# Kernel optimization log

Hardware: AMD Instinct MI355X
Metric: run time of the kernel (lower is better)

## Reference

```python
import jax, jax.numpy as jnp
import numpy as np
from jax.scipy.special import logsumexp

B, T, V, E, H, K = 64, 512, 21128, 256, 512, 31


def setup_inputs() -> dict:
    key = jax.random.key(0)
    ks = jax.random.split(key, 32)
    s = 1.0 / np.sqrt(H)

    def u(k, shape):
        return jax.random.uniform(k, shape, jnp.float32, -s, s)

    inp = {
        "input_ids": jax.random.randint(ks[0], (B, T), 0, V),
        "labels": jax.random.randint(ks[1], (B, T), 0, K),
        "emb": jax.random.normal(ks[2], (V, E), jnp.float32) * 0.05,
    }
    i = 3
    for layer, insz in (("l0", E), ("l1", 2 * H)):
        for d in ("f", "b"):
            inp["w_ih_%s%s" % (layer, d)] = u(ks[i], (3 * H, insz)); i += 1
            inp["w_hh_%s%s" % (layer, d)] = u(ks[i], (3 * H, H)); i += 1
            inp["b_ih_%s%s" % (layer, d)] = u(ks[i], (3 * H,)); i += 1
            inp["b_hh_%s%s" % (layer, d)] = u(ks[i], (3 * H,)); i += 1
    inp["cls_w"] = u(ks[i], (K, 2 * H))
    inp["cls_b"] = u(ks[i + 1], (K,))
    inp["crf_start"] = jax.random.normal(ks[i + 2], (K,), jnp.float32) * 0.1
    inp["crf_end"] = jax.random.normal(ks[i + 3], (K,), jnp.float32) * 0.1
    inp["crf_trans"] = jax.random.normal(ks[i + 4], (K, K), jnp.float32) * 0.1
    return inp


def gru_dir(x, w_ih, w_hh, b_ih, b_hh, reverse):
    # x: [B, T, in]. PyTorch GRU gate math, gates ordered (r, z, n).
    xp = jnp.einsum('bti,gi->btg', x, w_ih) + b_ih  # [B, T, 3H] precomputed input gates
    if reverse:
        xp = xp[:, ::-1]
    h0 = jnp.zeros((x.shape[0], w_hh.shape[1]), x.dtype)

    def step(h, xt):
        gh = h @ w_hh.T + b_hh
        xr, xz, xn = jnp.split(xt, 3, axis=-1)
        hr, hz, hn = jnp.split(gh, 3, axis=-1)
        r = jax.nn.sigmoid(xr + hr)
        z = jax.nn.sigmoid(xz + hz)
        n = jnp.tanh(xn + r * hn)
        h_new = (1.0 - z) * n + z * h
        return h_new, h_new

    _, hs = jax.lax.scan(step, h0, jnp.swapaxes(xp, 0, 1))
    hs = jnp.swapaxes(hs, 0, 1)  # [B, T, H]
    if reverse:
        hs = hs[:, ::-1]
    return hs


def crf_llh(emissions, tags, mask, start, end, trans):
    # Linear-chain CRF log-likelihood, summed over batch. mask[:, 0] assumed True.
    Bn = emissions.shape[0]
    mf = mask.astype(emissions.dtype)
    bidx = jnp.arange(Bn)
    em_t = jnp.take_along_axis(emissions, tags[:, :, None], axis=2)[:, :, 0]  # [B, T]
    num = start[tags[:, 0]] + em_t[:, 0]
    tr = trans[tags[:, :-1], tags[:, 1:]]  # [B, T-1]
    num = num + jnp.sum((tr + em_t[:, 1:]) * mf[:, 1:], axis=1)
    last_idx = jnp.sum(mask.astype(jnp.int32), axis=1) - 1
    num = num + end[tags[bidx, last_idx]]

    alpha0 = start[None, :] + emissions[:, 0]  # [B, K]

    def step(alpha, inp):
        em, m = inp  # em [B, K], m [B]
        nxt = logsumexp(alpha[:, :, None] + trans[None] + em[:, None, :], axis=1)
        return jnp.where(m[:, None], nxt, alpha), None

    alpha, _ = jax.lax.scan(
        step, alpha0,
        (jnp.swapaxes(emissions[:, 1:], 0, 1), jnp.swapaxes(mask[:, 1:], 0, 1)))
    denom = logsumexp(alpha + end[None, :], axis=1)
    return jnp.sum(num - denom)


def reference(input_ids, labels, emb,
              w_ih_l0f, w_hh_l0f, b_ih_l0f, b_hh_l0f,
              w_ih_l0b, w_hh_l0b, b_ih_l0b, b_hh_l0b,
              w_ih_l1f, w_hh_l1f, b_ih_l1f, b_hh_l1f,
              w_ih_l1b, w_hh_l1b, b_ih_l1b, b_hh_l1b,
              cls_w, cls_b, crf_start, crf_end, crf_trans):
    x = emb[input_ids]  # [B, T, E]
    f0 = gru_dir(x, w_ih_l0f, w_hh_l0f, b_ih_l0f, b_hh_l0f, False)
    b0 = gru_dir(x, w_ih_l0b, w_hh_l0b, b_ih_l0b, b_hh_l0b, True)
    h1 = jnp.concatenate([f0, b0], axis=-1)  # [B, T, 2H]
    f1 = gru_dir(h1, w_ih_l1f, w_hh_l1f, b_ih_l1f, b_hh_l1f, False)
    b1 = gru_dir(h1, w_ih_l1b, w_hh_l1b, b_ih_l1b, b_hh_l1b, True)
    gru_out = jnp.concatenate([f1, b1], axis=-1)  # [B, T, 2H]
    emissions = jnp.einsum('bth,kh->btk', gru_out, cls_w) + cls_b  # [B, T, K]
    mask = labels > -1  # labels.gt(labels_padding_value=-1)
    loss = -crf_llh(emissions, labels, mask, crf_start, crf_end, crf_trans)
    return (loss, emissions)
```

## Files before the change

kernel.cpp:

```cpp
#include <hip/hip_runtime.h>

#define DI __device__ __forceinline__

constexpr int B_  = 64;
constexpr int T_  = 512;
constexpr int E_  = 256;
constexpr int H_  = 512;
constexpr int G_  = 1536;
constexpr int H2_ = 1024;
constexpr int K_  = 31;
constexpr int BT_ = B_ * T_;
constexpr int TC_ = 64;
constexpr int NC_ = T_ / TC_;

typedef float        f32x4  __attribute__((ext_vector_type(4)));
typedef short        bf16x8 __attribute__((ext_vector_type(8)));
typedef unsigned int u32x4  __attribute__((ext_vector_type(4)));
typedef unsigned long long ull;

DI float bf2f(unsigned short u) {
    union { unsigned int i; float f; } v; v.i = ((unsigned int)u) << 16; return v.f;
}
DI unsigned short f2bf(float f) {
    union { float f; unsigned int i; } v; v.f = f;
    unsigned int r = v.i + 0x7fffu + ((v.i >> 16) & 1u);
    return (unsigned short)(r >> 16);
}
DI float sigm(float x) { return 1.f / (1.f + __expf(-x)); }
DI float tanh_(float x) {
    x = fminf(15.f, fmaxf(-15.f, x));
    float e = __expf(-2.f * x);
    return (1.f - e) / (1.f + e);
}

#define MFMA16(a, b, c) __builtin_amdgcn_mfma_f32_16x16x32_bf16(a, b, c, 0, 0, 0)

__global__ void cvt_f32_bf16(const float* __restrict__ src, unsigned short* __restrict__ dst, int n) {
    int i = blockIdx.x * blockDim.x + threadIdx.x;
    int stride = gridDim.x * blockDim.x;
    for (; i < n; i += stride) dst[i] = f2bf(src[i]);
}

__global__ __launch_bounds__(256) void cvt_cls(const float* __restrict__ src,
                                               unsigned short* __restrict__ dstf,
                                               unsigned short* __restrict__ dstb) {
    int i = blockIdx.x * 256 + threadIdx.x;
    if (i >= 32 * H_) return;
    int n = i >> 9, k = i & 511;
    float vf = (n < K_) ? src[n * H2_ + k] : 0.f;
    float vb = (n < K_) ? src[n * H2_ + H_ + k] : 0.f;
    dstf[i] = f2bf(vf);
    dstb[i] = f2bf(vb);
}

__global__ __launch_bounds__(256) void emis_bias_init(const float* __restrict__ cls_b,
                                                      float* __restrict__ out1) {
    int i = blockIdx.x * 256 + threadIdx.x;
    int stride = gridDim.x * 256;
    for (; i < BT_ * K_; i += stride) {
        int n = i - (i / K_) * K_;
        out1[i] = cls_b[n];
    }
}

template <bool OUTF32, bool ACCUM, bool WF32, bool AGATHER>
DI void gemm_tile(unsigned short (*As)[40], unsigned short (*Ws)[40],
                  const unsigned short* A, const float* gsrc, const int* ids, int lda,
                  size_t arow0, const void* W, int ldw, int nrows, int n0,
                  const float* bias, void* Cout, int ldc, size_t crow0,
                  int nout, int ksz, int tid) {
    const int w = tid >> 6, l = tid & 63;
    const int srow = tid >> 2, sc8 = (tid & 3) * 8;
    const int mw = (w >> 1) * 32, nw = (w & 1) * 32;
    const int fl = l & 15, fk = (l >> 4) * 8;
    f32x4 z4 = { 0.f, 0.f, 0.f, 0.f };
    f32x4 acc[2][2];
    acc[0][0] = z4; acc[0][1] = z4; acc[1][0] = z4; acc[1][1] = z4;
    size_t abase;
    if (AGATHER) abase = (size_t)ids[arow0 + srow] * lda;
    else         abase = (arow0 + srow) * (size_t)lda;

    for (int kc = 0; kc < ksz; kc += 32) {
        u32x4 av, wvv;
        if (AGATHER) {
            const float4* ap = (const float4*)(gsrc + abase + kc + sc8);
            float4 a0 = ap[0], a1 = ap[1];
            union { unsigned short s[8]; u32x4 v; } r;
            r.s[0] = f2bf(a0.x); r.s[1] = f2bf(a0.y); r.s[2] = f2bf(a0.z); r.s[3] = f2bf(a0.w);
            r.s[4] = f2bf(a1.x); r.s[5] = f2bf(a1.y); r.s[6] = f2bf(a1.z); r.s[7] = f2bf(a1.w);
            av = r.v;
        } else {
            av = *(const u32x4*)(A + abase + kc + sc8);
        }
        if (WF32) {
            const float4* wp = (const float4*)((const float*)W + (size_t)(n0 + srow) * ldw + kc + sc8);
            float4 w0 = wp[0], w1 = wp[1];
            union { unsigned short s[8]; u32x4 v; } r;
            r.s[0] = f2bf(w0.x); r.s[1] = f2bf(w0.y); r.s[2] = f2bf(w0.z); r.s[3] = f2bf(w0.w);
            r.s[4] = f2bf(w1.x); r.s[5] = f2bf(w1.y); r.s[6] = f2bf(w1.z); r.s[7] = f2bf(w1.w);
            wvv = r.v;
        } else {
            if (n0 + srow < nrows)
                wvv = *(const u32x4*)((const unsigned short*)W + (size_t)(n0 + srow) * ldw + kc + sc8);
            else { u32x4 zz = { 0u, 0u, 0u, 0u }; wvv = zz; }
        }
        __syncthreads();
        *(u32x4*)&As[srow][sc8] = av;
        *(u32x4*)&Ws[srow][sc8] = wvv;
        __syncthreads();
        bf16x8 a0 = *(const bf16x8*)&As[mw + fl][fk];
        bf16x8 a1 = *(const bf16x8*)&As[mw + 16 + fl][fk];
        bf16x8 b0 = *(const bf16x8*)&Ws[nw + fl][fk];
        bf16x8 b1 = *(const bf16x8*)&Ws[nw + 16 + fl][fk];
        acc[0][0] = MFMA16(a0, b0, acc[0][0]);
        acc[0][1] = MFMA16(a0, b1, acc[0][1]);
        acc[1][0] = MFMA16(a1, b0, acc[1][0]);
        acc[1][1] = MFMA16(a1, b1, acc[1][1]);
    }

    #pragma unroll
    for (int mf = 0; mf < 2; ++mf)
        #pragma unroll
        for (int nf = 0; nf < 2; ++nf) {
            int col = n0 + nw + nf * 16 + fl;
            if (col >= nout) continue;
            float bv = bias ? bias[col] : 0.f;
            #pragma unroll
            for (int j = 0; j < 4; ++j) {
                int r = mw + mf * 16 + (l >> 4) * 4 + j;
                size_t crow = crow0 + r;
                float v = acc[mf][nf][j] + bv;
                if (OUTF32) {
                    float* C = (float*)Cout;
                    if (ACCUM) C[crow * ldc + col] += v;
                    else       C[crow * ldc + col] = v;
                } else {
                    ((unsigned short*)Cout)[crow * ldc + col] = f2bf(v);
                }
            }
        }
}

template <bool OUTF32, bool ACCUM, bool WF32, bool AGATHER>
__global__ __launch_bounds__(256) void gemm_k(
        const unsigned short* __restrict__ A, const float* __restrict__ gsrc,
        const int* __restrict__ ids, int lda, int m_base, int astride,
        const void* __restrict__ W, int ldw, int nrows,
        const float* __restrict__ bias,
        void* __restrict__ Cout, int ldc, int c_base, int cstride, int nout, int ksz) {
    __shared__ unsigned short As[64][40];
    __shared__ unsigned short Ws[64][40];
    gemm_tile<OUTF32, ACCUM, WF32, AGATHER>(As, Ws, A, gsrc, ids, lda,
        (size_t)m_base + (size_t)blockIdx.x * astride, W, ldw, nrows,
        blockIdx.y * 64, bias, Cout, ldc,
        (size_t)c_base + (size_t)blockIdx.x * cstride, nout, ksz, threadIdx.x);
}

__global__ __launch_bounds__(256) void emis_k(
        const unsigned short* __restrict__ gof, const unsigned short* __restrict__ gob,
        const unsigned short* __restrict__ clsf, const unsigned short* __restrict__ clsb,
        float* __restrict__ out1, int t0f, int t0b) {
    __shared__ unsigned short As[64][40];
    __shared__ unsigned short Ws[64][40];
    const unsigned short* A = blockIdx.y ? gob : gof;
    const unsigned short* W = blockIdx.y ? clsb : clsf;
    int t0 = blockIdx.y ? t0b : t0f;
    gemm_tile<true, true, false, false>(As, Ws, A, nullptr, nullptr, H_,
        (size_t)blockIdx.x * TC_, W, H_, 32, 0, nullptr,
        (void*)out1, K_, (size_t)t0 + (size_t)blockIdx.x * T_, K_, H_, threadIdx.x);
}

template <bool AGATHER>
__global__ __launch_bounds__(256, 1) void fused_scan_gemm(
        int c, int layer,
        const unsigned short* __restrict__ xpc_f, const unsigned short* __restrict__ xpc_b,
        const unsigned short* __restrict__ whh_f, const unsigned short* __restrict__ whh_b,
        const float* __restrict__ bhh_f, const float* __restrict__ bhh_b,
        unsigned int* __restrict__ hpub,
        float* __restrict__ hcar,
        unsigned short* __restrict__ out_f, unsigned short* __restrict__ out_b,
        int ldo, int mode, int* __restrict__ flags,
        const unsigned short* __restrict__ gA, const float* __restrict__ gsrc,
        const int* __restrict__ gids, int glda,
        const float* __restrict__ gwf, const float* __restrict__ gwb,
        const float* __restrict__ gbf, const float* __restrict__ gbb,
        unsigned short* __restrict__ xpf_nxt, unsigned short* __restrict__ xpb_nxt,
        int t0f_n, int t0b_n, int do_gemm) {
    __shared__ unsigned short As[64][40];
    __shared__ unsigned short Ws[64][40];
    __shared__ unsigned short hs[16 * 512];
    const int bid = blockIdx.x;
    const int tid = threadIdx.x;

    if (bid >= 64) {
        if (!do_gemm) return;
        const int gb = bid - 64;
        for (int job = gb; job < 2 * 64 * 24; job += 192) {
            int dirj = job & 1;
            int rest = job >> 1;
            int mt = rest & 63;
            int nt = rest >> 6;
            const float* gw = dirj ? gwb : gwf;
            const float* gbias = dirj ? gbb : gbf;
            unsigned short* gout = dirj ? xpb_nxt : xpf_nxt;
            int t0 = dirj ? t0b_n : t0f_n;
            gemm_tile<false, false, true, AGATHER>(As, Ws, gA, gsrc, gids, glda,
                (size_t)t0 + (size_t)mt * T_, gw, glda, G_, nt * 64, gbias,
                (void*)gout, G_, (size_t)mt * TC_, G_, glda, tid);
        }
        return;
    }

    const int dir = bid >> 5;
    const int rb  = bid & 31;
    const int ug  = rb >> 2;
    const int bg  = rb & 3;
    const int w = tid >> 6, l = tid & 63;
    const int fl = l & 15, q = l >> 4, fko = q * 8;
    const unsigned short* xp = dir ? xpc_b : xpc_f;
    const unsigned short* whh = dir ? whh_b : whh_f;
    const float* bhh = dir ? bhh_b : bhh_f;
    unsigned short* outp = dir ? out_b : out_f;
    int* pollb  = flags + (dir * 4 + bg) * 8 * 32;
    int* myflag = pollb + ug * 32;

    const int u0w = ug * 64 + w * 16;
    bf16x8 wv[3][16];
    #pragma unroll
    for (int g = 0; g < 3; ++g)
        #pragma unroll
        for (int ks = 0; ks < 16; ++ks)
            wv[g][ks] = *(const bf16x8*)(whh + (size_t)(g * H_ + u0w + fl) * H_ + ks * 32 + fko);

    const int u = u0w + fl;
    const float br_ = bhh[u], bz_ = bhh[H_ + u], bn_ = bhh[2 * H_ + u];
    const int mb = bg * 16 + q * 4;
    const int srowl = tid >> 4;
    const int sseg  = tid & 15;

    float hp[4];
    if (c > 0) {
        #pragma unroll
        for (int j = 0; j < 4; ++j) hp[j] = hcar[dir * (B_ * H_) + (mb + j) * H_ + u];
    } else {
        #pragma unroll
        for (int j = 0; j < 4; ++j) hp[j] = 0.f;
    }

    unsigned short xg[3][4];
    auto ldxp = [&](int tl) {
        #pragma unroll
        for (int j = 0; j < 4; ++j) {
            const unsigned short* xb = xp + ((size_t)((mb + j) * TC_ + tl) * G_) + u;
            xg[0][j] = xb[0]; xg[1][j] = xb[H_]; xg[2][j] = xb[2 * H_];
        }
    };
    ldxp(dir ? (TC_ - 1) : 0);

    for (int sl = 0; sl < TC_; ++sl) {
        const int s  = c * TC_ + sl;
        const int gs = layer * T_ + s;
        const int t = dir ? (T_ - 1 - s) : s;
        const int tloc = dir ? (TC_ - 1 - sl) : sl;

        f32x4 z4 = { 0.f, 0.f, 0.f, 0.f };
        f32x4 acc[3];
        acc[0] = z4; acc[1] = z4; acc[2] = z4;

        if (s > 0) {
            if (sl > 0) {
                int v = gs;
                if (l < 8) v = __hip_atomic_load(pollb + l * 32, __ATOMIC_RELAXED, __HIP_MEMORY_SCOPE_AGENT);
                while (!__all(v >= gs)) {
                    __builtin_amdgcn_s_sleep(1);
                    if (l < 8) v = __hip_atomic_load(pollb + l * 32, __ATOMIC_RELAXED, __HIP_MEMORY_SCOPE_AGENT);
                }
                asm volatile("" ::: "memory");
            }
            {
                const ull* src = (const ull*)(hpub
                    + ((size_t)((((s - 1) & 1) * 2 + dir) * B_ + bg * 16 + srowl)) * 256)
                    + sseg * 8;
                ull qv[8];
                #pragma unroll
                for (int i = 0; i < 8; ++i)
                    qv[i] = __hip_atomic_load(src + i, __ATOMIC_RELAXED, __HIP_MEMORY_SCOPE_AGENT);
                char* dst = (char*)hs + srowl * 1024;
                #pragma unroll
                for (int i = 0; i < 4; ++i) {
                    unsigned int byt = (unsigned int)(sseg * 64 + i * 16);
                    byt ^= ((unsigned int)(srowl & 7)) << 4;
                    union { ull qq[2]; u32x4 v4; } pk;
                    pk.qq[0] = qv[2 * i]; pk.qq[1] = qv[2 * i + 1];
                    *(u32x4*)(dst + byt) = pk.v4;
                }
            }
            __syncthreads();
            #pragma unroll
            for (int ks = 0; ks < 16; ++ks) {
                unsigned int byt = (unsigned int)(ks * 64 + q * 16);
                byt ^= ((unsigned int)(fl & 7)) << 4;
                bf16x8 afr = *(const bf16x8*)((const char*)hs + fl * 1024 + byt);
                acc[0] = MFMA16(afr, wv[0][ks], acc[0]);
                acc[1] = MFMA16(afr, wv[1][ks], acc[1]);
                acc[2] = MFMA16(afr, wv[2][ks], acc[2]);
            }
        }

        unsigned short hb16s[4];
        #pragma unroll
        for (int j = 0; j < 4; ++j) {
            float xr = bf2f(xg[0][j]);
            float xz = bf2f(xg[1][j]);
            float xn = bf2f(xg[2][j]);
            float r = sigm(xr + acc[0][j] + br_);
            float z = sigm(xz + acc[1][j] + bz_);
            float nn = tanh_(xn + r * (acc[2][j] + bn_));
            float hv = (1.f - z) * nn + z * hp[j];
            hp[j] = hv;
            hb16s[j] = f2bf(hv);
        }

        unsigned int* hw = hpub + (size_t)((s & 1) * 2 + dir) * (B_ * 256);
        #pragma unroll
        for (int j = 0; j < 4; ++j) {
            unsigned int pv = (unsigned int)(unsigned short)__shfl_xor((int)hb16s[j], 1);
            if ((fl & 1) == 0) {
                unsigned int pk32 = (unsigned int)hb16s[j] | (pv << 16);
                __hip_atomic_store(hw + (size_t)(mb + j) * 256 + (u >> 1), pk32,
                                   __ATOMIC_RELAXED, __HIP_MEMORY_SCOPE_AGENT);
            }
        }
        asm volatile("" ::: "memory");
        #pragma unroll
        for (int j = 0; j < 4; ++j) {
            size_t row = mode ? (size_t)((mb + j) * TC_ + tloc) : ((size_t)(mb + j) * T_ + t);
            outp[row * ldo + u] = hb16s[j];
        }
        if (sl < TC_ - 1) ldxp(dir ? (TC_ - 2 - sl) : (sl + 1));
        asm volatile("s_waitcnt vmcnt(16)" ::: "memory");
        __builtin_amdgcn_s_barrier();
        if (tid == 0)
            __hip_atomic_store(myflag, gs + 1, __ATOMIC_RELAXED, __HIP_MEMORY_SCOPE_AGENT);
    }

    #pragma unroll
    for (int j = 0; j < 4; ++j) hcar[dir * (B_ * H_) + (mb + j) * H_ + u] = hp[j];
}

__global__ __launch_bounds__(64) void crf_kernel(const float* __restrict__ em,
                                                 const int* __restrict__ labels,
                                                 const float* __restrict__ start,
                                                 const float* __restrict__ endv,
                                                 const float* __restrict__ trans,
                                                 float* __restrict__ partials) {
    __shared__ float tr[32 * 32];
    const int b = blockIdx.x, l = threadIdx.x;
    for (int e2 = l; e2 < 961; e2 += 64) {
        int r = e2 / 31, cc = e2 - r * 31;
        tr[r * 32 + cc] = trans[e2];
    }
    if (l < 32) tr[31 * 32 + l] = 0.f;
    __syncthreads();
    const int* lab = labels + b * T_;
    const float* eb = em + (size_t)b * T_ * K_;

    float part = 0.f, cnt = 0.f;
    for (int t = l; t < T_; t += 64) {
        int lt = lab[t];
        if (lt > -1) {
            cnt += 1.f;
            if (t > 0) part += tr[lab[t - 1] * 32 + lt] + eb[t * K_ + lt];
        }
    }
    #pragma unroll
    for (int o = 32; o; o >>= 1) { part += __shfl_xor(part, o); cnt += __shfl_xor(cnt, o); }
    int lastidx = (int)cnt - 1;
    float num = part + start[lab[0]] + eb[lab[0]] + endv[lab[lastidx]];

    const int jj = l & 31, half = l >> 5;
    const int i0 = half * 16;
    const int ecol = (jj < K_) ? jj : (K_ - 1);
    float a = (jj < K_) ? (start[jj] + eb[jj]) : -3.0e38f;
    for (int t = 1; t < T_; ++t) {
        float tv[16];
        float m = -3.0e38f;
        #pragma unroll
        for (int k = 0; k < 16; ++k) {
            float av = __shfl(a, i0 + k);
            float x = av + tr[(i0 + k) * 32 + jj];
            tv[k] = x;
            m = fmaxf(m, x);
        }
        float ss = 0.f;
        #pragma unroll
        for (int k = 0; k < 16; ++k) ss += __expf(tv[k] - m);
        float m2 = __shfl_xor(m, 32), s2 = __shfl_xor(ss, 32);
        float M = fmaxf(m, m2);
        float S = ss * __expf(m - M) + s2 * __expf(m2 - M);
        float anew = eb[t * K_ + ecol] + M + __logf(S);
        a = ((lab[t] > -1) && (jj < K_)) ? anew : a;
    }
    float v = (jj < K_) ? (a + endv[jj]) : -3.0e38f;
    float m = v;
    #pragma unroll
    for (int o = 32; o; o >>= 1) m = fmaxf(m, __shfl_xor(m, o));
    float ss = (half == 0 && jj < K_) ? __expf(v - m) : 0.f;
    #pragma unroll
    for (int o = 32; o; o >>= 1) ss += __shfl_xor(ss, o);
    if (l == 0) partials[b] = num - (m + __logf(ss));
}

__global__ __launch_bounds__(64) void loss_reduce(const float* __restrict__ partials,
                                                  float* __restrict__ out) {
    float v = partials[threadIdx.x];
    #pragma unroll
    for (int o = 32; o; o >>= 1) v += __shfl_xor(v, o);
    if (threadIdx.x == 0) out[0] = -v;
}

__global__ void sentinel(float* __restrict__ out, float v) { out[0] = -v; }

extern "C" void kernel_launch(void* const* d_in, const int* in_sizes, int n_in,
                              void* d_out, int out_size, void* d_ws, size_t ws_size,
                              hipStream_t stream) {
    const int*   ids      = (const int*)d_in[0];
    const int*   labels   = (const int*)d_in[1];
    const float* emb      = (const float*)d_in[2];
    const float* wih[4]   = { (const float*)d_in[3], (const float*)d_in[7], (const float*)d_in[11], (const float*)d_in[15] };
    const float* whh[4]   = { (const float*)d_in[4], (const float*)d_in[8], (const float*)d_in[12], (const float*)d_in[16] };
    const float* bih[4]   = { (const float*)d_in[5], (const float*)d_in[9], (const float*)d_in[13], (const float*)d_in[17] };
    const float* bhh[4]   = { (const float*)d_in[6], (const float*)d_in[10], (const float*)d_in[14], (const float*)d_in[18] };
    const float* cls_w    = (const float*)d_in[19];
    const float* cls_b    = (const float*)d_in[20];
    const float* c_start  = (const float*)d_in[21];
    const float* c_end    = (const float*)d_in[22];
    const float* c_trans  = (const float*)d_in[23];
    float* out = (float*)d_out;
    float* out1 = out + 1;

    char* p = (char*)d_ws;
    size_t used = 0;
    auto alloc = [&](size_t bytes) -> char* {
        char* r = p;
        size_t a = (bytes + 255) & ~(size_t)255;
        p += a; used += a;
        return r;
    };
    unsigned short* xpF[2]; unsigned short* xpB[2];
    for (int i = 0; i < 2; ++i) {
        xpF[i] = (unsigned short*)alloc((size_t)B_ * TC_ * G_ * 2);
        xpB[i] = (unsigned short*)alloc((size_t)B_ * TC_ * G_ * 2);
    }
    unsigned short* h1   = (unsigned short*)alloc((size_t)BT_ * H2_ * 2);
    unsigned short* gof  = (unsigned short*)alloc((size_t)B_ * TC_ * H_ * 2);
    unsigned short* gob  = (unsigned short*)alloc((size_t)B_ * TC_ * H_ * 2);
    unsigned short* clsf  = (unsigned short*)alloc((size_t)32 * H_ * 2);
    unsigned short* clshb = (unsigned short*)alloc((size_t)32 * H_ * 2);
    unsigned short* whhbf = (unsigned short*)alloc((size_t)G_ * H_ * 2);
    unsigned short* whhbb = (unsigned short*)alloc((size_t)G_ * H_ * 2);
    unsigned int*   hpub  = (unsigned int*)alloc((size_t)2 * 2 * B_ * 256 * 4);
    float*          hcar  = (float*)alloc((size_t)2 * B_ * H_ * 4);
    float*          partials = (float*)alloc((size_t)B_ * 4);
    int*            flags = (int*)alloc((size_t)2 * 4 * 8 * 32 * 4);

    if (used > ws_size) {
        sentinel<<<dim3(1), dim3(1), 0, stream>>>(out, (float)(ws_size >> 20));
        return;
    }

    hipMemsetAsync(flags, 0, (size_t)2 * 4 * 8 * 32 * 4, stream);
    cvt_cls<<<dim3((32 * H_ + 255) / 256), dim3(256), 0, stream>>>(cls_w, clsf, clshb);
    emis_bias_init<<<dim3(1024), dim3(256), 0, stream>>>(cls_b, out1);

    for (int layer = 0; layer < 2; ++layer) {
        const float* wf  = wih[layer * 2 + 0];
        const float* wb  = wih[layer * 2 + 1];
        const float* bf_ = bih[layer * 2 + 0];
        const float* bb_ = bih[layer * 2 + 1];
        const float* bhf = bhh[layer * 2 + 0];
        const float* bhb = bhh[layer * 2 + 1];

        cvt_f32_bf16<<<dim3(2048), dim3(256), 0, stream>>>(whh[layer * 2 + 0], whhbf, G_ * H_);
        cvt_f32_bf16<<<dim3(2048), dim3(256), 0, stream>>>(whh[layer * 2 + 1], whhbb, G_ * H_);

        if (layer == 0) {
            gemm_k<false, false, true, true><<<dim3(64, 24), dim3(256), 0, stream>>>(
                nullptr, emb, ids, E_, 0, T_, wf, E_, G_, bf_, (void*)xpF[0], G_, 0, TC_, G_, E_);
            gemm_k<false, false, true, true><<<dim3(64, 24), dim3(256), 0, stream>>>(
                nullptr, emb, ids, E_, T_ - TC_, T_, wb, E_, G_, bb_, (void*)xpB[0], G_, 0, TC_, G_, E_);
        } else {
            gemm_k<false, false, true, false><<<dim3(64, 24), dim3(256), 0, stream>>>(
                h1, nullptr, nullptr, H2_, 0, T_, wf, H2_, G_, bf_, (void*)xpF[0], G_, 0, TC_, G_, H2_);
            gemm_k<false, false, true, false><<<dim3(64, 24), dim3(256), 0, stream>>>(
                h1, nullptr, nullptr, H2_, T_ - TC_, T_, wb, H2_, G_, bb_, (void*)xpB[0], G_, 0, TC_, G_, H2_);
        }

        for (int c = 0; c < NC_; ++c) {
            int dg = (c + 1 < NC_) ? 1 : 0;
            int t0f_n = (c + 1) * TC_;
            int t0b_n = T_ - (c + 2) * TC_;
            if (layer == 0) {
                fused_scan_gemm<true><<<dim3(256), dim3(256), 0, stream>>>(
                    c, 0, xpF[c & 1], xpB[c & 1], whhbf, whhbb, bhf, bhb, hpub, hcar,
                    h1, h1 + H_, H2_, 0, flags,
                    nullptr, emb, ids, E_, wf, wb, bf_, bb_,
                    xpF[(c + 1) & 1], xpB[(c + 1) & 1], t0f_n, t0b_n, dg);
            } else {
                fused_scan_gemm<false><<<dim3(256), dim3(256), 0, stream>>>(
                    c, 1, xpF[c & 1], xpB[c & 1], whhbf, whhbb, bhf, bhb, hpub, hcar,
                    gof, gob, H_, 1, flags,
                    h1, nullptr, nullptr, H2_, wf, wb, bf_, bb_,
                    xpF[(c + 1) & 1], xpB[(c + 1) & 1], t0f_n, t0b_n, dg);
                int t0f = c * TC_;
                int t0b = T_ - (c + 1) * TC_;
                emis_k<<<dim3(64, 2), dim3(256), 0, stream>>>(gof, gob, clsf, clshb, out1, t0f, t0b);
            }
        }
    }

    crf_kernel<<<dim3(B_), dim3(64), 0, stream>>>(out1, labels, c_start, c_end, c_trans, partials);
    loss_reduce<<<dim3(1), dim3(64), 0, stream>>>(partials, out);
}
```

Measured before the change: 4.322 ms.

## Per-wave step flags with double-buffered LDS, larger side GEMM tiles

In the recurrent scan, each wave now publishes its own progress flag and pollers wait on 32 per-wave flags instead of 8 per-block flags. This lets the end-of-step block barrier be dropped, and the hidden-state staging in LDS is double-buffered by step parity so waves can move ahead safely. Separately, for layer 1 the co-scheduled input-projection GEMM blocks use a 128x128 tile per job with fp32 weights converted inline, replacing the shared 64x64 gemm_tile path. The aim is to cut barrier stalls on the serial critical path and to make the overlapped GEMM more efficient, at the cost of more flag polling traffic and added LDS and register pressure.

```diff
diff --git a/kernel.cpp b/kernel.cpp
--- a/kernel.cpp
+++ b/kernel.cpp
@@ -186,27 +186,102 @@
         const float* __restrict__ gbf, const float* __restrict__ gbb,
         unsigned short* __restrict__ xpf_nxt, unsigned short* __restrict__ xpb_nxt,
         int t0f_n, int t0b_n, int do_gemm) {
-    __shared__ unsigned short As[64][40];
-    __shared__ unsigned short Ws[64][40];
-    __shared__ unsigned short hs[16 * 512];
+    __shared__ __align__(16) char smem[32768];
     const int bid = blockIdx.x;
     const int tid = threadIdx.x;
 
     if (bid >= 64) {
         if (!do_gemm) return;
         const int gb = bid - 64;
-        for (int job = gb; job < 2 * 64 * 24; job += 192) {
-            int dirj = job & 1;
-            int rest = job >> 1;
-            int mt = rest & 63;
-            int nt = rest >> 6;
-            const float* gw = dirj ? gwb : gwf;
-            const float* gbias = dirj ? gbb : gbf;
-            unsigned short* gout = dirj ? xpb_nxt : xpf_nxt;
-            int t0 = dirj ? t0b_n : t0f_n;
-            gemm_tile<false, false, true, AGATHER>(As, Ws, gA, gsrc, gids, glda,
-                (size_t)t0 + (size_t)mt * T_, gw, glda, G_, nt * 64, gbias,
-                (void*)gout, G_, (size_t)mt * TC_, G_, glda, tid);
+        if (AGATHER) {
+            unsigned short (*As)[40] = (unsigned short (*)[40])smem;
+            unsigned short (*Ws)[40] = (unsigned short (*)[40])(smem + 5120);
+            for (int job = gb; job < 2 * 64 * 24; job += 192) {
+                int dirj = job & 1;
+                int rest = job >> 1;
+                int mt = rest & 63;
+                int nt = rest >> 6;
+                const float* gw = dirj ? gwb : gwf;
+                const float* gbias = dirj ? gbb : gbf;
+                unsigned short* gout = dirj ? xpb_nxt : xpf_nxt;
+                int t0 = dirj ? t0b_n : t0f_n;
+                gemm_tile<false, false, true, true>(As, Ws, gA, gsrc, gids, glda,
+                    (size_t)t0 + (size_t)mt * T_, gw, glda, G_, nt * 64, gbias,
+                    (void*)gout, G_, (size_t)mt * TC_, G_, glda, tid);
+            }
+        } else {
+            unsigned short (*A1)[40] = (unsigned short (*)[40])smem;
+            unsigned short (*W1)[40] = (unsigned short (*)[40])(smem + 10240);
+            const int w = tid >> 6, l = tid & 63;
+            const int fl = l & 15, fk = (l >> 4) * 8;
+            const int mw2 = (w >> 1) * 64, nw2 = (w & 1) * 64;
+            const int rA = tid >> 1, ch = (tid & 1) * 16;
+            #pragma unroll 1
+            for (int it = 0; it < 4; ++it) {
+                int job = gb * 4 + it;
+                int dirj = (job >= 384) ? 1 : 0;
+                int jj = job - dirj * 384;
+                int nt = jj >> 5;
+                int mt2 = jj & 31;
+                const float* gw = dirj ? gwb : gwf;
+                const float* gbias = dirj ? gbb : gbf;
+                unsigned short* gout = dirj ? xpb_nxt : xpf_nxt;
+                int t0 = dirj ? t0b_n : t0f_n;
+                int n0j = nt * 128;
+                const int mA = mt2 * 2 + (rA >> 6), tlA = rA & 63;
+                const unsigned short* aRow = gA + ((size_t)mA * T_ + t0 + tlA) * H2_ + ch;
+                const float* wRow = gw + (size_t)(n0j + rA) * H2_ + ch;
+                f32x4 z4 = { 0.f, 0.f, 0.f, 0.f };
+                f32x4 acc[4][4];
+                #pragma unroll
+                for (int a2 = 0; a2 < 4; ++a2)
+                    #pragma unroll
+                    for (int b2 = 0; b2 < 4; ++b2) acc[a2][b2] = z4;
+
+                for (int kc = 0; kc < H2_; kc += 32) {
+                    u32x4 av0 = *(const u32x4*)(aRow + kc);
+                    u32x4 av1 = *(const u32x4*)(aRow + kc + 8);
+                    float4 w0 = *(const float4*)(wRow + kc);
+                    float4 w1 = *(const float4*)(wRow + kc + 4);
+                    float4 w2 = *(const float4*)(wRow + kc + 8);
+                    float4 w3 = *(const float4*)(wRow + kc + 12);
+                    union { unsigned short s[8]; u32x4 v; } r0, r1;
+                    r0.s[0] = f2bf(w0.x); r0.s[1] = f2bf(w0.y); r0.s[2] = f2bf(w0.z); r0.s[3] = f2bf(w0.w);
+                    r0.s[4] = f2bf(w1.x); r0.s[5] = f2bf(w1.y); r0.s[6] = f2bf(w1.z); r0.s[7] = f2bf(w1.w);
+                    r1.s[0] = f2bf(w2.x); r1.s[1] = f2bf(w2.y); r1.s[2] = f2bf(w2.z); r1.s[3] = f2bf(w2.w);
+                    r1.s[4] = f2bf(w3.x); r1.s[5] = f2bf(w3.y); r1.s[6] = f2bf(w3.z); r1.s[7] = f2bf(w3.w);
+                    __syncthreads();
+                    *(u32x4*)&A1[rA][ch] = av0;
+                    *(u32x4*)&A1[rA][ch + 8] = av1;
+                    *(u32x4*)&W1[rA][ch] = r0.v;
+                    *(u32x4*)&W1[rA][ch + 8] = r1.v;
+                    __syncthreads();
+                    bf16x8 af[4], bf[4];
+                    #pragma unroll
+                    for (int a2 = 0; a2 < 4; ++a2) af[a2] = *(const bf16x8*)&A1[mw2 + a2 * 16 + fl][fk];
+                    #pragma unroll
+                    for (int b2 = 0; b2 < 4; ++b2) bf[b2] = *(const bf16x8*)&W1[nw2 + b2 * 16 + fl][fk];
+                    #pragma unroll
+                    for (int a2 = 0; a2 < 4; ++a2)
+                        #pragma unroll
+                        for (int b2 = 0; b2 < 4; ++b2)
+                            acc[a2][b2] = MFMA16(af[a2], bf[b2], acc[a2][b2]);
+                }
+
+                #pragma unroll
+                for (int a2 = 0; a2 < 4; ++a2)
+                    #pragma unroll
+                    for (int b2 = 0; b2 < 4; ++b2) {
+                        int col = n0j + nw2 + b2 * 16 + fl;
+                        float bv = gbias[col];
+                        #pragma unroll
+                        for (int j = 0; j < 4; ++j) {
+                            int rloc = mw2 + a2 * 16 + (l >> 4) * 4 + j;
+                            int m = mt2 * 2 + (rloc >> 6), tl = rloc & 63;
+                            gout[((size_t)m * TC_ + tl) * G_ + col] = f2bf(acc[a2][b2][j] + bv);
+                        }
+                    }
+            }
         }
         return;
     }
@@ -221,8 +296,8 @@
     const unsigned short* whh = dir ? whh_b : whh_f;
     const float* bhh = dir ? bhh_b : bhh_f;
     unsigned short* outp = dir ? out_b : out_f;
-    int* pollb  = flags + (dir * 4 + bg) * 8 * 32;
-    int* myflag = pollb + ug * 32;
+    int* pollb  = flags + (dir * 4 + bg) * 32 * 32;
+    int* myflag = pollb + (ug * 4 + w) * 32;
 
     const int u0w = ug * 64 + w * 16;
     bf16x8 wv[3][16];
@@ -268,12 +343,13 @@
         acc[0] = z4; acc[1] = z4; acc[2] = z4;
 
         if (s > 0) {
+            const unsigned int rpar = (unsigned int)(((s - 1) & 1) * 16384);
             if (sl > 0) {
                 int v = gs;
-                if (l < 8) v = __hip_atomic_load(pollb + l * 32, __ATOMIC_RELAXED, __HIP_MEMORY_SCOPE_AGENT);
+                if (l < 32) v = __hip_atomic_load(pollb + l * 32, __ATOMIC_RELAXED, __HIP_MEMORY_SCOPE_AGENT);
                 while (!__all(v >= gs)) {
                     __builtin_amdgcn_s_sleep(1);
-                    if (l < 8) v = __hip_atomic_load(pollb + l * 32, __ATOMIC_RELAXED, __HIP_MEMORY_SCOPE_AGENT);
+                    if (l < 32) v = __hip_atomic_load(pollb + l * 32, __ATOMIC_RELAXED, __HIP_MEMORY_SCOPE_AGENT);
                 }
                 asm volatile("" ::: "memory");
             }
@@ -285,7 +361,7 @@
                 #pragma unroll
                 for (int i = 0; i < 8; ++i)
                     qv[i] = __hip_atomic_load(src + i, __ATOMIC_RELAXED, __HIP_MEMORY_SCOPE_AGENT);
-                char* dst = (char*)hs + srowl * 1024;
+                char* dst = smem + rpar + srowl * 1024;
                 #pragma unroll
                 for (int i = 0; i < 4; ++i) {
                     unsigned int byt = (unsigned int)(sseg * 64 + i * 16);
@@ -300,7 +376,7 @@
             for (int ks = 0; ks < 16; ++ks) {
                 unsigned int byt = (unsigned int)(ks * 64 + q * 16);
                 byt ^= ((unsigned int)(fl & 7)) << 4;
-                bf16x8 afr = *(const bf16x8*)((const char*)hs + fl * 1024 + byt);
+                bf16x8 afr = *(const bf16x8*)(smem + rpar + fl * 1024 + byt);
                 acc[0] = MFMA16(afr, wv[0][ks], acc[0]);
                 acc[1] = MFMA16(afr, wv[1][ks], acc[1]);
                 acc[2] = MFMA16(afr, wv[2][ks], acc[2]);
@@ -339,8 +415,7 @@
         }
         if (sl < TC_ - 1) ldxp(dir ? (TC_ - 2 - sl) : (sl + 1));
         asm volatile("s_waitcnt vmcnt(16)" ::: "memory");
-        __builtin_amdgcn_s_barrier();
-        if (tid == 0)
+        if (l == 0)
             __hip_atomic_store(myflag, gs + 1, __ATOMIC_RELAXED, __HIP_MEMORY_SCOPE_AGENT);
     }
 
@@ -462,14 +537,14 @@
     unsigned int*   hpub  = (unsigned int*)alloc((size_t)2 * 2 * B_ * 256 * 4);
     float*          hcar  = (float*)alloc((size_t)2 * B_ * H_ * 4);
     float*          partials = (float*)alloc((size_t)B_ * 4);
-    int*            flags = (int*)alloc((size_t)2 * 4 * 8 * 32 * 4);
+    int*            flags = (int*)alloc((size_t)2 * 4 * 32 * 32 * 4);
 
     if (used > ws_size) {
         sentinel<<<dim3(1), dim3(1), 0, stream>>>(out, (float)(ws_size >> 20));
         return;
     }
 
-    hipMemsetAsync(flags, 0, (size_t)2 * 4 * 8 * 32 * 4, stream);
+    hipMemsetAsync(flags, 0, (size_t)2 * 4 * 32 * 32 * 4, stream);
     cvt_cls<<<dim3((32 * H_ + 255) / 256), dim3(256), 0, stream>>>(cls_w, clsf, clshb);
     emis_bias_init<<<dim3(1024), dim3(256), 0, stream>>>(cls_b, out1);
 
```

Measured after the change: 4.300 ms. No clear change (-0.5%).
